# Kernel tuning notes

Hardware: AMD Instinct MI355X
Metric: run time of the kernel (lower is better)

## Reference

```python
import jax, jax.numpy as jnp
import numpy as np

T = 10
CH, H, W = 16, 16, 264  # torch grid_sample sees view(1,16,16,264) as N,C,H,W
L, C = 256, 264


def _warp(img, pose):
    """Replicates F.affine_grid + F.grid_sample (bilinear, zeros padding,
    align_corners=False) on img of shape (CH,H,W) with pose=(dx,dy,dyaw)."""
    dx, dy, yaw = pose[0], pose[1], pose[2]
    cos, sin = jnp.cos(yaw), jnp.sin(yaw)
    # normalized base grid, align_corners=False: (2i+1)/N - 1
    xs = (2.0 * jnp.arange(W, dtype=img.dtype) + 1.0) / W - 1.0  # (W,)
    ys = (2.0 * jnp.arange(H, dtype=img.dtype) + 1.0) / H - 1.0  # (H,)
    gx = cos * xs[None, :] + sin * ys[:, None] + dx   # (H,W)
    gy = -sin * xs[None, :] + cos * ys[:, None] + dy  # (H,W)
    # unnormalize (align_corners=False)
    ix = ((gx + 1.0) * W - 1.0) * 0.5
    iy = ((gy + 1.0) * H - 1.0) * 0.5
    ix0 = jnp.floor(ix); iy0 = jnp.floor(iy)
    ix1 = ix0 + 1.0;     iy1 = iy0 + 1.0
    wx1 = ix - ix0; wx0 = 1.0 - wx1
    wy1 = iy - iy0; wy0 = 1.0 - wy1

    def gather(xf, yf):
        inb = (xf >= 0) & (xf < W) & (yf >= 0) & (yf < H)
        xi = jnp.clip(xf.astype(jnp.int32), 0, W - 1)
        yi = jnp.clip(yf.astype(jnp.int32), 0, H - 1)
        v = img[:, yi, xi]                      # (CH,H,W)
        return v * inb.astype(img.dtype)        # zero padding

    out = (gather(ix0, iy0) * (wx0 * wy0)
           + gather(ix1, iy0) * (wx1 * wy0)
           + gather(ix0, iy1) * (wx0 * wy1)
           + gather(ix1, iy1) * (wx1 * wy1))
    return out  # (CH,H,W)


def _forward(fuse_feature, delta_ego_pos):
    ff = fuse_feature                              # (10,256,264)
    dp = delta_ego_pos                             # (10,3)
    ff_sp = ff.reshape(T, CH, H, W)
    # prefix sums: P[k] = sum(dp[0:k]); cumulative pose for (b,t) = -sum(dp[t-1:b])
    P = jnp.concatenate([jnp.zeros((1, 3), dp.dtype), jnp.cumsum(dp, axis=0)], axis=0)
    bs = jnp.repeat(jnp.arange(T), T - 1)          # (90,) frame index
    ts = jnp.tile(jnp.arange(1, T), T)             # (90,) past-frame offset t in [1,9]
    poses = -(P[bs] - P[ts - 1])                   # (90,3)
    valid = (ts <= bs)                             # n_valid_past(b) = b
    src = ff_sp[ts]                                # (90,CH,H,W)
    warped = jax.vmap(_warp)(src, poses)           # (90,CH,H,W)
    warped = warped * valid[:, None, None, None].astype(ff.dtype)
    aligned = jnp.zeros((T, T, CH, H, W), ff.dtype)
    aligned = aligned.at[bs, (T - 1) - ts].set(warped)
    aligned = aligned.at[:, T - 1].set(ff_sp)      # current frame, unwarped
    # (B,T,L*C) self-attention fusion
    tb = aligned.reshape(T, T, L * C)
    scores = jnp.einsum('btd,bsd->bts', tb, tb)
    attn = jax.nn.softmax(scores, axis=-1)
    fused = jnp.einsum('bts,bsd->btd', attn, tb)
    fused = fused.mean(axis=1)                     # (B, L*C)
    return fused.reshape(T, L, C)                  # (10,256,264)


def setup_inputs() -> dict:
    key = jax.random.key(0)
    k1, k2 = jax.random.split(key)
    # scale features so the d=67584 dot products don't saturate the softmax
    fuse_feature = jax.random.normal(k1, (T, L, C), dtype=jnp.float32) * 0.02
    delta_ego_pos = jax.random.normal(k2, (T, 3), dtype=jnp.float32) * 0.1
    return {"fuse_feature": fuse_feature, "delta_ego_pos": delta_ego_pos}


def reference(fuse_feature, delta_ego_pos):
    return _forward(fuse_feature, delta_ego_pos)
```

## Files before the change

kernel.cpp:

```cpp
#include <hip/hip_runtime.h>
#include <math.h>

#define TT 10
#define CHN 16
#define HH 16
#define WW 264
#define HW (HH*WW)
#define DD (CHN*HW)
#define NCH 66
#define NACC 55


__device__ __forceinline__ void pose_setup(const float* __restrict__ dp, int b,
                                           float4* __restrict__ pose) {
    if (threadIdx.x < TT-1) {
        int ts = (int)threadIdx.x + 1;
        float ax = 0.f, ay = 0.f, az = 0.f;
        for (int j = 0; j < ts-1; ++j) { ax += dp[3*j]; ay += dp[3*j+1]; az += dp[3*j+2]; }
        float bx = 0.f, by = 0.f, bz = 0.f;
        for (int j = 0; j < b; ++j)    { bx += dp[3*j]; by += dp[3*j+1]; bz += dp[3*j+2]; }
        float yaw = az - bz;
        pose[threadIdx.x] = make_float4(ax - bx, ay - by,
                                        (float)cos((double)yaw), (float)sin((double)yaw));
    }
}

__device__ __forceinline__ void plan_slot(float xs, float ys, float4 m,
                                          int& o00, int& o10, int& o01, int& o11,
                                          float& w00, float& w10, float& w01, float& w11) {
    float gx =  m.z*xs + m.w*ys + m.x;
    float gy = -m.w*xs + m.z*ys + m.y;
    float ix = ((gx + 1.f)*(float)WW - 1.f)*0.5f;
    float iy = ((gy + 1.f)*(float)HH - 1.f)*0.5f;
    float ix0f = floorf(ix), iy0f = floorf(iy);
    float wx1 = ix - ix0f, wx0 = 1.f - wx1;
    float wy1 = iy - iy0f, wy0 = 1.f - wy1;
    int ix0 = (int)ix0f, iy0 = (int)iy0f;
    int ix1 = ix0 + 1,   iy1 = iy0 + 1;
    bool inx0 = (ix0 >= 0) && (ix0 < WW);
    bool inx1 = (ix1 >= 0) && (ix1 < WW);
    bool iny0 = (iy0 >= 0) && (iy0 < HH);
    bool iny1 = (iy1 >= 0) && (iy1 < HH);
    int xi0 = min(max(ix0, 0), WW-1), xi1 = min(max(ix1, 0), WW-1);
    int yi0 = min(max(iy0, 0), HH-1), yi1 = min(max(iy1, 0), HH-1);
    float wx0m = inx0 ? wx0 : 0.f, wx1m = inx1 ? wx1 : 0.f;
    float wy0m = iny0 ? wy0 : 0.f, wy1m = iny1 ? wy1 : 0.f;
    o00 = yi0*WW + xi0; o10 = yi0*WW + xi1;
    o01 = yi1*WW + xi0; o11 = yi1*WW + xi1;
    w00 = wx0m*wy0m; w10 = wx1m*wy0m;
    w01 = wx0m*wy1m; w11 = wx1m*wy1m;
}

__device__ __forceinline__ int tri_idx(int a0, int a1) {
    return a0*TT - a0*(a0-1)/2 + (a1 - a0);
}

__global__ __launch_bounds__(256) void gram_kernel(const float* __restrict__ ff,
                                                   const float* __restrict__ dp,
                                                   float* __restrict__ scores) {
    int b = blockIdx.y;
    int chunk = blockIdx.x >> 1, cgrp = blockIdx.x & 1;
    int lane = threadIdx.x & 63, wv = threadIdx.x >> 6;
    int ch0 = cgrp*8 + wv*2;
    int p = chunk*64 + lane;
    __shared__ float4 pose[TT-1];
    pose_setup(dp, b, pose);
    __syncthreads();

    int y = p / WW, x = p - y*WW;
    float xs = (2.f*(float)x + 1.f)*(1.f/(float)WW) - 1.f;
    float ys = (2.f*(float)y + 1.f)*(1.f/(float)HH) - 1.f;

    float v[TT][2];
    #pragma unroll
    for (int s = 0; s < TT; ++s) {
        #pragma unroll
        for (int c = 0; c < 2; ++c) v[s][c] = 0.f;
        if (s == TT-1) {
            const float* src = ff + b*DD + ch0*HW + p;
            #pragma unroll
            for (int c = 0; c < 2; ++c) v[s][c] = src[c*HW];
            continue;
        }
        int ts = (TT-1) - s;
        if (ts > b) continue;
        int o00,o10,o01,o11; float w00,w10,w01,w11;
        plan_slot(xs, ys, pose[ts-1], o00,o10,o01,o11, w00,w10,w01,w11);
        const float* src = ff + ts*DD + ch0*HW;
        #pragma unroll
        for (int c = 0; c < 2; ++c) {
            const float* fc = src + c*HW;
            v[s][c] = fc[o00]*w00 + fc[o10]*w10 + fc[o01]*w01 + fc[o11]*w11;
        }
    }

    float acc[NACC];
    #pragma unroll
    for (int k = 0; k < NACC; ++k) acc[k] = 0.f;
    #pragma unroll
    for (int c = 0; c < 2; ++c) {
        int k = 0;
        #pragma unroll
        for (int t = 0; t < TT; ++t)
            #pragma unroll
            for (int s2 = t; s2 < TT; ++s2)
                acc[k++] += v[t][c]*v[s2][c];
    }

    __shared__ float red[NACC*4];
    #pragma unroll
    for (int k = 0; k < NACC; ++k) {
        float a = acc[k];
        #pragma unroll
        for (int o = 32; o > 0; o >>= 1) a += __shfl_down(a, o);
        if (lane == 0) red[k*4 + wv] = a;
    }
    __syncthreads();
    if (threadIdx.x < NACC) {
        float a = red[threadIdx.x*4] + red[threadIdx.x*4+1]
                + red[threadIdx.x*4+2] + red[threadIdx.x*4+3];
        atomicAdd(&scores[b*NACC + threadIdx.x], a);
    }
}

__global__ __launch_bounds__(256) void out_kernel(const float* __restrict__ ff,
                                                  const float* __restrict__ dp,
                                                  const float* __restrict__ scores,
                                                  float* __restrict__ out) {
    int b = blockIdx.y;
    int chunk = blockIdx.x >> 1, cgrp = blockIdx.x & 1;
    int lane = threadIdx.x & 63, wv = threadIdx.x >> 6;
    int ch0 = cgrp*8 + wv*2;
    int p = chunk*64 + lane;
    __shared__ float4 pose[TT-1];
    __shared__ float sc[NACC];
    __shared__ float mx_l[TT], den_l[TT];
    __shared__ float wl[TT];
    pose_setup(dp, b, pose);
    if (threadIdx.x >= 64 && threadIdx.x < 64 + NACC)
        sc[threadIdx.x - 64] = scores[b*NACC + (threadIdx.x - 64)];
    __syncthreads();
    if (threadIdx.x < TT) {
        int t = threadIdx.x;
        float mx = -1e30f;
        #pragma unroll
        for (int s = 0; s < TT; ++s) {
            int a0 = min(t, s), a1 = max(t, s);
            mx = fmaxf(mx, sc[tri_idx(a0, a1)]);
        }
        float den = 0.f;
        #pragma unroll
        for (int s = 0; s < TT; ++s) {
            int a0 = min(t, s), a1 = max(t, s);
            den += expf(sc[tri_idx(a0, a1)] - mx);
        }
        mx_l[t] = mx; den_l[t] = den;
    }
    __syncthreads();
    if (threadIdx.x < TT) {
        int s = threadIdx.x;
        float a2 = 0.f;
        #pragma unroll
        for (int t = 0; t < TT; ++t) {
            int a0 = min(t, s), a1 = max(t, s);
            a2 += expf(sc[tri_idx(a0, a1)] - mx_l[t]) / den_l[t];
        }
        wl[s] = a2 * 0.1f;
    }
    __syncthreads();

    int y = p / WW, x = p - y*WW;
    float xs = (2.f*(float)x + 1.f)*(1.f/(float)WW) - 1.f;
    float ys = (2.f*(float)y + 1.f)*(1.f/(float)HH) - 1.f;

    float o[2] = {0.f, 0.f};
    #pragma unroll
    for (int s = 0; s < TT; ++s) {
        if (s == TT-1) {
            float wb = wl[s];
            const float* src = ff + b*DD + ch0*HW + p;
            #pragma unroll
            for (int c = 0; c < 2; ++c) o[c] += wb*src[c*HW];
            continue;
        }
        int ts = (TT-1) - s;
        if (ts > b) continue;
        int o00,o10,o01,o11; float w00,w10,w01,w11;
        plan_slot(xs, ys, pose[ts-1], o00,o10,o01,o11, w00,w10,w01,w11);
        float wb = wl[s];
        w00 *= wb; w10 *= wb; w01 *= wb; w11 *= wb;
        const float* src = ff + ts*DD + ch0*HW;
        #pragma unroll
        for (int c = 0; c < 2; ++c) {
            const float* fc = src + c*HW;
            o[c] += fc[o00]*w00 + fc[o10]*w10 + fc[o01]*w01 + fc[o11]*w11;
        }
    }
    #pragma unroll
    for (int c = 0; c < 2; ++c)
        out[(size_t)b*DD + (ch0 + c)*HW + p] = o[c];
}

extern "C" void kernel_launch(void* const* d_in, const int* in_sizes, int n_in,
                              void* d_out, int out_size, void* d_ws, size_t ws_size,
                              hipStream_t stream) {
    const float* ff = (const float*)d_in[0];
    const float* dp = (const float*)d_in[1];
    float* out = (float*)d_out;

    float* scores = (float*)d_ws;

    gram_kernel<<<dim3(NCH*2, TT), 256, 0, stream>>>(ff, dp, scores);
    out_kernel <<<dim3(NCH*2, TT), 256, 0, stream>>>(ff, dp, scores, out);
}
```

Before: 103.9 us.

## Replace score atomics with per-block partials and branch-free masked warp loops

The gram kernel now writes each block's 55 partial dot products into a strided workspace instead of atomically adding into a shared scores array. The output kernel sums the 132 partials per frame before computing the softmax weights. This removes atomic contention and also the dependence on a zeroed workspace. Separately, the per-slot validity branch is replaced by zeroing the bilinear weights, so every thread issues all gathers unconditionally. That adds memory loads for the invalid past frames in exchange for uniform control flow.

Result: slower. 139.9 us (+34.7%).

```diff
diff --git a/kernel.cpp b/kernel.cpp
--- a/kernel.cpp
+++ b/kernel.cpp
@@ -9,6 +9,8 @@
 #define DD (CHN*HW)
 #define NCH 66
 #define NACC 55
+#define NPART (NCH*2)
+#define PSTRIDE 56
 
 
 __device__ __forceinline__ void pose_setup(const float* __restrict__ dp, int b,
@@ -57,9 +59,10 @@
 
 __global__ __launch_bounds__(256) void gram_kernel(const float* __restrict__ ff,
                                                    const float* __restrict__ dp,
-                                                   float* __restrict__ scores) {
+                                                   float* __restrict__ part) {
     int b = blockIdx.y;
-    int chunk = blockIdx.x >> 1, cgrp = blockIdx.x & 1;
+    int j = blockIdx.x;
+    int chunk = j >> 1, cgrp = j & 1;
     int lane = threadIdx.x & 63, wv = threadIdx.x >> 6;
     int ch0 = cgrp*8 + wv*2;
     int p = chunk*64 + lane;
@@ -72,20 +75,18 @@
     float ys = (2.f*(float)y + 1.f)*(1.f/(float)HH) - 1.f;
 
     float v[TT][2];
-    #pragma unroll
-    for (int s = 0; s < TT; ++s) {
-        #pragma unroll
-        for (int c = 0; c < 2; ++c) v[s][c] = 0.f;
-        if (s == TT-1) {
-            const float* src = ff + b*DD + ch0*HW + p;
-            #pragma unroll
-            for (int c = 0; c < 2; ++c) v[s][c] = src[c*HW];
-            continue;
-        }
+    {
+        const float* src = ff + b*DD + ch0*HW + p;
+        v[TT-1][0] = src[0];
+        v[TT-1][1] = src[HW];
+    }
+    #pragma unroll
+    for (int s = 0; s < TT-1; ++s) {
         int ts = (TT-1) - s;
-        if (ts > b) continue;
         int o00,o10,o01,o11; float w00,w10,w01,w11;
         plan_slot(xs, ys, pose[ts-1], o00,o10,o01,o11, w00,w10,w01,w11);
+        float vm = (ts <= b) ? 1.f : 0.f;
+        w00 *= vm; w10 *= vm; w01 *= vm; w11 *= vm;
         const float* src = ff + ts*DD + ch0*HW;
         #pragma unroll
         for (int c = 0; c < 2; ++c) {
@@ -119,16 +120,17 @@
     if (threadIdx.x < NACC) {
         float a = red[threadIdx.x*4] + red[threadIdx.x*4+1]
                 + red[threadIdx.x*4+2] + red[threadIdx.x*4+3];
-        atomicAdd(&scores[b*NACC + threadIdx.x], a);
+        part[(size_t)(b*NPART + j)*PSTRIDE + threadIdx.x] = a;
     }
 }
 
 __global__ __launch_bounds__(256) void out_kernel(const float* __restrict__ ff,
                                                   const float* __restrict__ dp,
-                                                  const float* __restrict__ scores,
+                                                  const float* __restrict__ part,
                                                   float* __restrict__ out) {
     int b = blockIdx.y;
-    int chunk = blockIdx.x >> 1, cgrp = blockIdx.x & 1;
+    int j = blockIdx.x;
+    int chunk = j >> 1, cgrp = j & 1;
     int lane = threadIdx.x & 63, wv = threadIdx.x >> 6;
     int ch0 = cgrp*8 + wv*2;
     int p = chunk*64 + lane;
@@ -137,8 +139,14 @@
     __shared__ float mx_l[TT], den_l[TT];
     __shared__ float wl[TT];
     pose_setup(dp, b, pose);
-    if (threadIdx.x >= 64 && threadIdx.x < 64 + NACC)
-        sc[threadIdx.x - 64] = scores[b*NACC + (threadIdx.x - 64)];
+    if (threadIdx.x >= 64 && threadIdx.x < 64 + NACC) {
+        int k = threadIdx.x - 64;
+        const float* pp = part + (size_t)b*NPART*PSTRIDE + k;
+        float s = 0.f;
+        #pragma unroll 4
+        for (int jj = 0; jj < NPART; ++jj) s += pp[(size_t)jj*PSTRIDE];
+        sc[k] = s;
+    }
     __syncthreads();
     if (threadIdx.x < TT) {
         int t = threadIdx.x;
@@ -173,21 +181,19 @@
     float xs = (2.f*(float)x + 1.f)*(1.f/(float)WW) - 1.f;
     float ys = (2.f*(float)y + 1.f)*(1.f/(float)HH) - 1.f;
 
-    float o[2] = {0.f, 0.f};
-    #pragma unroll
-    for (int s = 0; s < TT; ++s) {
-        if (s == TT-1) {
-            float wb = wl[s];
-            const float* src = ff + b*DD + ch0*HW + p;
-            #pragma unroll
-            for (int c = 0; c < 2; ++c) o[c] += wb*src[c*HW];
-            continue;
-        }
+    float o[2];
+    {
+        float wb = wl[TT-1];
+        const float* src = ff + b*DD + ch0*HW + p;
+        o[0] = wb*src[0];
+        o[1] = wb*src[HW];
+    }
+    #pragma unroll
+    for (int s = 0; s < TT-1; ++s) {
         int ts = (TT-1) - s;
-        if (ts > b) continue;
         int o00,o10,o01,o11; float w00,w10,w01,w11;
         plan_slot(xs, ys, pose[ts-1], o00,o10,o01,o11, w00,w10,w01,w11);
-        float wb = wl[s];
+        float wb = (ts <= b) ? wl[s] : 0.f;
         w00 *= wb; w10 *= wb; w01 *= wb; w11 *= wb;
         const float* src = ff + ts*DD + ch0*HW;
         #pragma unroll
@@ -208,8 +214,8 @@
     const float* dp = (const float*)d_in[1];
     float* out = (float*)d_out;
 
-    float* scores = (float*)d_ws;
-
-    gram_kernel<<<dim3(NCH*2, TT), 256, 0, stream>>>(ff, dp, scores);
-    out_kernel <<<dim3(NCH*2, TT), 256, 0, stream>>>(ff, dp, scores, out);
-}
+    float* part = (float*)d_ws;
+
+    gram_kernel<<<dim3(NPART, TT), 256, 0, stream>>>(ff, dp, part);
+    out_kernel <<<dim3(NPART, TT), 256, 0, stream>>>(ff, dp, part, out);
+}
```

## Process four channels per wave and stage pose inputs in shared memory

Applied to the files above, without the earlier changes.

Each wave now handles four channels instead of two, halving the grid so each block covers all 16 channels for a 64-pixel chunk. The bilinear sample plan (offsets and weights) is amortized over more channel loads, and there are half as many partial-score atomics. Pose deltas are staged in shared memory, and in out_kernel the pose and softmax setup now run concurrently in different waves. The tradeoff is fewer blocks (660) and more registers per thread (a 10x4 value array), which can reduce occupancy and latency hiding on the gathers.

Measured after the change: 83.78 us. -19.3%, faster.

```diff
diff --git a/kernel.cpp b/kernel.cpp
--- a/kernel.cpp
+++ b/kernel.cpp
@@ -11,18 +11,23 @@
 #define NACC 55
 
 
-__device__ __forceinline__ void pose_setup(const float* __restrict__ dp, int b,
-                                           float4* __restrict__ pose) {
+__device__ __forceinline__ void pose_setup_fast(const float* __restrict__ dp,
+                                                int b,
+                                                float* __restrict__ dp_sh,
+                                                float4* __restrict__ pose) {
+    if (threadIdx.x < 3*TT) dp_sh[threadIdx.x] = dp[threadIdx.x];
+    __syncthreads();
     if (threadIdx.x < TT-1) {
         int ts = (int)threadIdx.x + 1;
         float ax = 0.f, ay = 0.f, az = 0.f;
-        for (int j = 0; j < ts-1; ++j) { ax += dp[3*j]; ay += dp[3*j+1]; az += dp[3*j+2]; }
+        for (int j = 0; j < ts-1; ++j) { ax += dp_sh[3*j]; ay += dp_sh[3*j+1]; az += dp_sh[3*j+2]; }
         float bx = 0.f, by = 0.f, bz = 0.f;
-        for (int j = 0; j < b; ++j)    { bx += dp[3*j]; by += dp[3*j+1]; bz += dp[3*j+2]; }
+        for (int j = 0; j < b; ++j)    { bx += dp_sh[3*j]; by += dp_sh[3*j+1]; bz += dp_sh[3*j+2]; }
         float yaw = az - bz;
         pose[threadIdx.x] = make_float4(ax - bx, ay - by,
                                         (float)cos((double)yaw), (float)sin((double)yaw));
     }
+    __syncthreads();
 }
 
 __device__ __forceinline__ void plan_slot(float xs, float ys, float4 m,
@@ -59,36 +64,34 @@
                                                    const float* __restrict__ dp,
                                                    float* __restrict__ scores) {
     int b = blockIdx.y;
-    int chunk = blockIdx.x >> 1, cgrp = blockIdx.x & 1;
     int lane = threadIdx.x & 63, wv = threadIdx.x >> 6;
-    int ch0 = cgrp*8 + wv*2;
-    int p = chunk*64 + lane;
+    int p = blockIdx.x*64 + lane;
+    __shared__ float dp_sh[3*TT];
     __shared__ float4 pose[TT-1];
-    pose_setup(dp, b, pose);
-    __syncthreads();
+    pose_setup_fast(dp, b, dp_sh, pose);
 
     int y = p / WW, x = p - y*WW;
     float xs = (2.f*(float)x + 1.f)*(1.f/(float)WW) - 1.f;
     float ys = (2.f*(float)y + 1.f)*(1.f/(float)HH) - 1.f;
 
-    float v[TT][2];
+    float v[TT][4];
     #pragma unroll
     for (int s = 0; s < TT; ++s) {
         #pragma unroll
-        for (int c = 0; c < 2; ++c) v[s][c] = 0.f;
+        for (int c = 0; c < 4; ++c) v[s][c] = 0.f;
         if (s == TT-1) {
-            const float* src = ff + b*DD + ch0*HW + p;
+            const float* src = ff + b*DD + (wv*4)*HW + p;
             #pragma unroll
-            for (int c = 0; c < 2; ++c) v[s][c] = src[c*HW];
+            for (int c = 0; c < 4; ++c) v[s][c] = src[c*HW];
             continue;
         }
         int ts = (TT-1) - s;
         if (ts > b) continue;
         int o00,o10,o01,o11; float w00,w10,w01,w11;
         plan_slot(xs, ys, pose[ts-1], o00,o10,o01,o11, w00,w10,w01,w11);
-        const float* src = ff + ts*DD + ch0*HW;
-        #pragma unroll
-        for (int c = 0; c < 2; ++c) {
+        const float* src = ff + ts*DD + (wv*4)*HW;
+        #pragma unroll
+        for (int c = 0; c < 4; ++c) {
             const float* fc = src + c*HW;
             v[s][c] = fc[o00]*w00 + fc[o10]*w10 + fc[o01]*w01 + fc[o11]*w11;
         }
@@ -98,7 +101,7 @@
     #pragma unroll
     for (int k = 0; k < NACC; ++k) acc[k] = 0.f;
     #pragma unroll
-    for (int c = 0; c < 2; ++c) {
+    for (int c = 0; c < 4; ++c) {
         int k = 0;
         #pragma unroll
         for (int t = 0; t < TT; ++t)
@@ -128,20 +131,30 @@
                                                   const float* __restrict__ scores,
                                                   float* __restrict__ out) {
     int b = blockIdx.y;
-    int chunk = blockIdx.x >> 1, cgrp = blockIdx.x & 1;
     int lane = threadIdx.x & 63, wv = threadIdx.x >> 6;
-    int ch0 = cgrp*8 + wv*2;
-    int p = chunk*64 + lane;
+    int p = blockIdx.x*64 + lane;
+    __shared__ float dp_sh[3*TT];
     __shared__ float4 pose[TT-1];
     __shared__ float sc[NACC];
     __shared__ float mx_l[TT], den_l[TT];
     __shared__ float wl[TT];
-    pose_setup(dp, b, pose);
+
+    if (threadIdx.x < 3*TT) dp_sh[threadIdx.x] = dp[threadIdx.x];
     if (threadIdx.x >= 64 && threadIdx.x < 64 + NACC)
         sc[threadIdx.x - 64] = scores[b*NACC + (threadIdx.x - 64)];
     __syncthreads();
-    if (threadIdx.x < TT) {
-        int t = threadIdx.x;
+    if (threadIdx.x < TT-1) {
+        int ts = (int)threadIdx.x + 1;
+        float ax = 0.f, ay = 0.f, az = 0.f;
+        for (int j = 0; j < ts-1; ++j) { ax += dp_sh[3*j]; ay += dp_sh[3*j+1]; az += dp_sh[3*j+2]; }
+        float bx = 0.f, by = 0.f, bz = 0.f;
+        for (int j = 0; j < b; ++j)    { bx += dp_sh[3*j]; by += dp_sh[3*j+1]; bz += dp_sh[3*j+2]; }
+        float yaw = az - bz;
+        pose[threadIdx.x] = make_float4(ax - bx, ay - by,
+                                        (float)cos((double)yaw), (float)sin((double)yaw));
+    }
+    if (threadIdx.x >= 64 && threadIdx.x < 64 + TT) {
+        int t = threadIdx.x - 64;
         float mx = -1e30f;
         #pragma unroll
         for (int s = 0; s < TT; ++s) {
@@ -173,14 +186,14 @@
     float xs = (2.f*(float)x + 1.f)*(1.f/(float)WW) - 1.f;
     float ys = (2.f*(float)y + 1.f)*(1.f/(float)HH) - 1.f;
 
-    float o[2] = {0.f, 0.f};
+    float o[4] = {0.f, 0.f, 0.f, 0.f};
     #pragma unroll
     for (int s = 0; s < TT; ++s) {
         if (s == TT-1) {
             float wb = wl[s];
-            const float* src = ff + b*DD + ch0*HW + p;
+            const float* src = ff + b*DD + (wv*4)*HW + p;
             #pragma unroll
-            for (int c = 0; c < 2; ++c) o[c] += wb*src[c*HW];
+            for (int c = 0; c < 4; ++c) o[c] += wb*src[c*HW];
             continue;
         }
         int ts = (TT-1) - s;
@@ -189,16 +202,16 @@
         plan_slot(xs, ys, pose[ts-1], o00,o10,o01,o11, w00,w10,w01,w11);
         float wb = wl[s];
         w00 *= wb; w10 *= wb; w01 *= wb; w11 *= wb;
-        const float* src = ff + ts*DD + ch0*HW;
-        #pragma unroll
-        for (int c = 0; c < 2; ++c) {
+        const float* src = ff + ts*DD + (wv*4)*HW;
+        #pragma unroll
+        for (int c = 0; c < 4; ++c) {
             const float* fc = src + c*HW;
             o[c] += fc[o00]*w00 + fc[o10]*w10 + fc[o01]*w01 + fc[o11]*w11;
         }
     }
     #pragma unroll
-    for (int c = 0; c < 2; ++c)
-        out[(size_t)b*DD + (ch0 + c)*HW + p] = o[c];
+    for (int c = 0; c < 4; ++c)
+        out[(size_t)b*DD + (wv*4 + c)*HW + p] = o[c];
 }
 
 extern "C" void kernel_launch(void* const* d_in, const int* in_sizes, int n_in,
@@ -210,6 +223,6 @@
 
     float* scores = (float*)d_ws;
 
-    gram_kernel<<<dim3(NCH*2, TT), 256, 0, stream>>>(ff, dp, scores);
-    out_kernel <<<dim3(NCH*2, TT), 256, 0, stream>>>(ff, dp, scores, out);
-}
+    gram_kernel<<<dim3(NCH, TT), 256, 0, stream>>>(ff, dp, scores);
+    out_kernel <<<dim3(NCH, TT), 256, 0, stream>>>(ff, dp, scores, out);
+}
```
